# Performance work log

Measured on AMD Instinct MI355X. Metric: run time of the kernel, lower is better.

## Reference

```python
import jax, jax.numpy as jnp
import numpy as np

N_NODES = 100000
N_EDGES = 3200000
IN_Z = 32
PROJ_H = 64
LOOP_D = 32
DEC_H = 64


def setup_inputs() -> dict:
    key = jax.random.key(0)
    ks = jax.random.split(key, 10)
    z_mod = jax.random.normal(ks[0], (N_NODES, IN_Z), dtype=jnp.float32)
    edge_index = jax.random.randint(ks[1], (2, N_EDGES), 0, N_NODES, dtype=jnp.int64)
    # loop_proj: Linear(32->64), ReLU, Linear(64->32)
    w1 = jax.random.normal(ks[2], (IN_Z, PROJ_H), dtype=jnp.float32) / np.sqrt(IN_Z)
    b1 = jnp.zeros((PROJ_H,), dtype=jnp.float32)
    w2 = jax.random.normal(ks[3], (PROJ_H, LOOP_D), dtype=jnp.float32) / np.sqrt(PROJ_H)
    b2 = jnp.zeros((LOOP_D,), dtype=jnp.float32)
    # decoder: Linear(2*loop_dim -> dec_hidden), ReLU, Linear(dec_hidden -> 1)
    dw1 = jax.random.normal(ks[4], (2 * LOOP_D, DEC_H), dtype=jnp.float32) / np.sqrt(2 * LOOP_D)
    db1 = jnp.zeros((DEC_H,), dtype=jnp.float32)
    dw2 = jax.random.normal(ks[5], (DEC_H, 1), dtype=jnp.float32) / np.sqrt(DEC_H)
    db2 = jnp.zeros((1,), dtype=jnp.float32)
    return {"z_mod": z_mod, "edge_index": edge_index, "w1": w1, "b1": b1,
            "w2": w2, "b2": b2, "dw1": dw1, "db1": db1, "dw2": dw2, "db2": db2}


def reference(z_mod, edge_index, w1, b1, w2, b2, dw1, db1, dw2, db2):
    # loop_proj: z_mod -> z_loop  [N, loop_dim]
    h = jax.nn.relu(z_mod @ w1 + b1)
    z_loop = h @ w2 + b2
    # edge-wise decoder: gather, concat, MLP
    zi = z_loop[edge_index[0]]            # [E, loop_dim]
    zj = z_loop[edge_index[1]]            # [E, loop_dim]
    he = jnp.concatenate([zi, zj], axis=-1)  # [E, 2*loop_dim]
    he = jax.nn.relu(he @ dw1 + db1)         # [E, dec_hidden]
    logits = (he @ dw2 + db2)[..., 0]        # [E]
    return logits
```

## Files before the change

### kernel.cpp

```cpp
#include <hip/hip_runtime.h>


typedef short bfrag4 __attribute__((ext_vector_type(4)));
typedef short s16x8  __attribute__((ext_vector_type(8)));
typedef float f32x4v __attribute__((ext_vector_type(4)));

#define N_NODES 100000
#define N_EDGES 3200000

__device__ __forceinline__ unsigned short f2bf(float f) {
    unsigned int i = __float_as_uint(f);
    unsigned int r = i + 0x7FFFu + ((i >> 16) & 1u);
    return (unsigned short)(r >> 16);
}

__device__ __forceinline__ bfrag4 cvt4(float x0, float x1, float x2, float x3) {
    bfrag4 v;
    v[0] = (short)f2bf(x0);
    v[1] = (short)f2bf(x1);
    v[2] = (short)f2bf(x2);
    v[3] = (short)f2bf(x3);
    return v;
}

__global__ __launch_bounds__(256) void node_proj_kernel(
    const float* __restrict__ z_mod,
    const float* __restrict__ w1,
    const float* __restrict__ b1,
    const float* __restrict__ w2,
    const float* __restrict__ b2,
    unsigned short* __restrict__ z_loop)
{
    __shared__ unsigned short hbuf[4][16 * 72];

    const int tid  = threadIdx.x;
    const int wave = tid >> 6;
    const int lane = tid & 63;
    const int quad = lane >> 4;
    const int col  = lane & 15;

    bfrag4 bw1[2][4];
    float  bias1[4];
    for (int t = 0; t < 4; ++t) {
        const int n = col + 16 * t;
        for (int s = 0; s < 2; ++s)
            for (int j = 0; j < 4; ++j)
                bw1[s][t][j] = (short)f2bf(w1[(s * 16 + quad * 4 + j) * 64 + n]);
        bias1[t] = b1[n];
    }
    bfrag4 bw2[4][2];
    float  bias2[2];
    for (int t = 0; t < 2; ++t) {
        const int n = col + 16 * t;
        for (int s = 0; s < 4; ++s)
            for (int j = 0; j < 4; ++j)
                bw2[s][t][j] = (short)f2bf(w2[(s * 16 + quad * 4 + j) * 32 + n]);
        bias2[t] = b2[n];
    }

    unsigned short* hrow = &hbuf[wave][0];

    const int gwave  = blockIdx.x * 4 + wave;
    const int nwaves = gridDim.x * 4;
    const int ntiles = N_NODES / 16;

    for (int tile = gwave; tile < ntiles; tile += nwaves) {
        const int node0 = tile * 16;
        const float* zrow = z_mod + (size_t)(node0 + col) * 32;

        f32x4v za0 = *(const f32x4v*)(zrow + 0 * 16 + quad * 4);
        f32x4v za1 = *(const f32x4v*)(zrow + 1 * 16 + quad * 4);
        bfrag4 a10 = cvt4(za0[0], za0[1], za0[2], za0[3]);
        bfrag4 a11 = cvt4(za1[0], za1[1], za1[2], za1[3]);

        f32x4v acc[4];
        for (int t = 0; t < 4; ++t) {
            f32x4v c = {bias1[t], bias1[t], bias1[t], bias1[t]};
            c = __builtin_amdgcn_mfma_f32_16x16x16bf16_1k(a10, bw1[0][t], c, 0, 0, 0);
            c = __builtin_amdgcn_mfma_f32_16x16x16bf16_1k(a11, bw1[1][t], c, 0, 0, 0);
            acc[t] = c;
        }

        for (int t = 0; t < 4; ++t)
            for (int r = 0; r < 4; ++r) {
                float v = acc[t][r];
                v = v > 0.f ? v : 0.f;
                hrow[(quad * 4 + r) * 72 + (col + 16 * t)] = f2bf(v);
            }
        asm volatile("" ::: "memory");

        f32x4v acc2[2];
        for (int t = 0; t < 2; ++t)
            acc2[t] = (f32x4v){bias2[t], bias2[t], bias2[t], bias2[t]};
        for (int s = 0; s < 4; ++s) {
            bfrag4 a2 = *(const bfrag4*)(hrow + col * 72 + s * 16 + quad * 4);
            for (int t = 0; t < 2; ++t)
                acc2[t] = __builtin_amdgcn_mfma_f32_16x16x16bf16_1k(a2, bw2[s][t], acc2[t], 0, 0, 0);
        }
        asm volatile("" ::: "memory");

        for (int t = 0; t < 2; ++t)
            for (int r = 0; r < 4; ++r)
                z_loop[(size_t)(node0 + quad * 4 + r) * 32 + (col + 16 * t)] =
                    f2bf(acc2[t][r]);
    }
}

__global__ __launch_bounds__(256) void edge_dec_kernel(
    const int*            __restrict__ eidx,
    const unsigned short* __restrict__ z_loop,
    const float*          __restrict__ dw1,
    const float*          __restrict__ db1,
    const float*          __restrict__ dw2,
    const float*          __restrict__ db2,
    float* __restrict__ out)
{
    const int tid  = threadIdx.x;
    const int lane = tid & 63;
    const int quad = lane >> 4;
    const int col  = lane & 15;

    s16x8 aw[2][4];
    float bias1[4][4];
    float w2v[4][4];
    for (int mt = 0; mt < 4; ++mt) {
        const int h = 16 * mt + col;
        for (int s = 0; s < 2; ++s)
            for (int j = 0; j < 8; ++j)
                aw[s][mt][j] = (short)f2bf(dw1[(32 * s + quad * 8 + j) * 64 + h]);
        for (int r = 0; r < 4; ++r) {
            bias1[mt][r] = db1[16 * mt + quad * 4 + r];
            w2v[mt][r]   = dw2[16 * mt + quad * 4 + r];
        }
    }
    const float bias2 = db2[0];

    const int gwave  = blockIdx.x * 4 + (tid >> 6);
    const int nwaves = gridDim.x * 4;
    const int npairs = N_EDGES / 32;

    int sA = eidx[gwave * 32 + col];
    int sB = eidx[gwave * 32 + 16 + col];
    int dA = eidx[N_EDGES + gwave * 32 + col];
    int dB = eidx[N_EDGES + gwave * 32 + 16 + col];

    for (int p = gwave; p < npairs; p += nwaves) {
        const int e0 = p * 32;

        s16x8 gA0 = *(const s16x8*)(z_loop + (size_t)sA * 32 + quad * 8);
        s16x8 gA1 = *(const s16x8*)(z_loop + (size_t)dA * 32 + quad * 8);
        s16x8 gB0 = *(const s16x8*)(z_loop + (size_t)sB * 32 + quad * 8);
        s16x8 gB1 = *(const s16x8*)(z_loop + (size_t)dB * 32 + quad * 8);

        const int pn = p + nwaves;
        const int pc = pn < npairs ? pn : gwave;
        sA = eidx[pc * 32 + col];
        sB = eidx[pc * 32 + 16 + col];
        dA = eidx[N_EDGES + pc * 32 + col];
        dB = eidx[N_EDGES + pc * 32 + 16 + col];

        f32x4v accA[4], accB[4];
        for (int mt = 0; mt < 4; ++mt) {
            f32x4v c = {bias1[mt][0], bias1[mt][1], bias1[mt][2], bias1[mt][3]};
            c = __builtin_amdgcn_mfma_f32_16x16x32_bf16(aw[0][mt], gA0, c, 0, 0, 0);
            c = __builtin_amdgcn_mfma_f32_16x16x32_bf16(aw[1][mt], gA1, c, 0, 0, 0);
            accA[mt] = c;
        }
        for (int mt = 0; mt < 4; ++mt) {
            f32x4v c = {bias1[mt][0], bias1[mt][1], bias1[mt][2], bias1[mt][3]};
            c = __builtin_amdgcn_mfma_f32_16x16x32_bf16(aw[0][mt], gB0, c, 0, 0, 0);
            c = __builtin_amdgcn_mfma_f32_16x16x32_bf16(aw[1][mt], gB1, c, 0, 0, 0);
            accB[mt] = c;
        }

        float pA = 0.f, pB = 0.f;
        for (int mt = 0; mt < 4; ++mt)
            for (int r = 0; r < 4; ++r) {
                float vA = accA[mt][r]; vA = vA > 0.f ? vA : 0.f;
                float vB = accB[mt][r]; vB = vB > 0.f ? vB : 0.f;
                pA += vA * w2v[mt][r];
                pB += vB * w2v[mt][r];
            }
        pA += __shfl_xor(pA, 16, 64);
        pA += __shfl_xor(pA, 32, 64);
        pB += __shfl_xor(pB, 16, 64);
        pB += __shfl_xor(pB, 32, 64);

        if (lane < 32) {
            float v = (lane < 16 ? pA : pB) + bias2;
            out[e0 + lane] = v;
        }
    }
}

extern "C" void kernel_launch(void* const* d_in, const int* in_sizes, int n_in,
                              void* d_out, int out_size, void* d_ws, size_t ws_size,
                              hipStream_t stream) {
    const float* z_mod = (const float*)d_in[0];
    const int*   eidx  = (const int*)d_in[1];
    const float* w1    = (const float*)d_in[2];
    const float* b1    = (const float*)d_in[3];
    const float* w2    = (const float*)d_in[4];
    const float* b2    = (const float*)d_in[5];
    const float* dw1   = (const float*)d_in[6];
    const float* db1   = (const float*)d_in[7];
    const float* dw2   = (const float*)d_in[8];
    const float* db2   = (const float*)d_in[9];
    float*          out    = (float*)d_out;
    unsigned short* z_loop = (unsigned short*)d_ws;

    node_proj_kernel<<<512, 256, 0, stream>>>(z_mod, w1, b1, w2, b2, z_loop);
    edge_dec_kernel<<<2048, 256, 0, stream>>>(eidx, z_loop, dw1, db1, dw2, db2, out);
}
```

Before: 152.3 us.

## Quantize projected node embeddings to int8 with per-node scales for edge gathers

The node projection kernel now stores z_loop as int8 with a per-node absmax scale instead of bf16, staging the quantized rows through shared memory for a coalesced write. The edge decoder gathers 8-byte int8 chunks plus a scale per endpoint and dequantizes to bf16 in registers before the MFMA. This halves the bytes of the random embedding gathers, at the cost of extra ALU work for dequantization, an additional scale gather per endpoint, and reduced numerical precision.

```diff
diff --git a/kernel.cpp b/kernel.cpp
--- a/kernel.cpp
+++ b/kernel.cpp
@@ -23,13 +23,31 @@
     return v;
 }
 
+__device__ __forceinline__ s16x8 dq8(long g, float s) {
+    int lo = (int)g;
+    int hi = (int)(g >> 32);
+    s16x8 o;
+#pragma unroll
+    for (int j = 0; j < 4; ++j) {
+        int bj = (lo << (24 - 8 * j)) >> 24;
+        o[j] = (short)f2bf((float)bj * s);
+    }
+#pragma unroll
+    for (int j = 0; j < 4; ++j) {
+        int bj = (hi << (24 - 8 * j)) >> 24;
+        o[4 + j] = (short)f2bf((float)bj * s);
+    }
+    return o;
+}
+
 __global__ __launch_bounds__(256) void node_proj_kernel(
     const float* __restrict__ z_mod,
     const float* __restrict__ w1,
     const float* __restrict__ b1,
     const float* __restrict__ w2,
     const float* __restrict__ b2,
-    unsigned short* __restrict__ z_loop)
+    char*  __restrict__ z8,
+    float* __restrict__ scales)
 {
     __shared__ unsigned short hbuf[4][16 * 72];
 
@@ -99,20 +117,40 @@
         }
         asm volatile("" ::: "memory");
 
-        for (int t = 0; t < 2; ++t)
+        float am[4];
+        for (int r = 0; r < 4; ++r)
+            am[r] = fmaxf(fabsf(acc2[0][r]), fabsf(acc2[1][r]));
+        for (int mask = 1; mask <= 8; mask <<= 1)
             for (int r = 0; r < 4; ++r)
-                z_loop[(size_t)(node0 + quad * 4 + r) * 32 + (col + 16 * t)] =
-                    f2bf(acc2[t][r]);
+                am[r] = fmaxf(am[r], __shfl_xor(am[r], mask, 64));
+
+        char* hb = (char*)hrow;
+        for (int r = 0; r < 4; ++r) {
+            const float inv = 127.f / fmaxf(am[r], 1e-30f);
+            for (int t = 0; t < 2; ++t) {
+                int q = (int)rintf(acc2[t][r] * inv);
+                hb[(quad * 4 + r) * 32 + (col + 16 * t)] = (char)q;
+            }
+        }
+        if (col == 0)
+            for (int r = 0; r < 4; ++r)
+                scales[node0 + quad * 4 + r] = am[r] * (1.f / 127.f);
+        asm volatile("" ::: "memory");
+
+        *(unsigned long long*)(z8 + (size_t)node0 * 32 + lane * 8) =
+            *(const unsigned long long*)(hb + lane * 8);
+        asm volatile("" ::: "memory");
     }
 }
 
 __global__ __launch_bounds__(256) void edge_dec_kernel(
-    const int*            __restrict__ eidx,
-    const unsigned short* __restrict__ z_loop,
-    const float*          __restrict__ dw1,
-    const float*          __restrict__ db1,
-    const float*          __restrict__ dw2,
-    const float*          __restrict__ db2,
+    const int*   __restrict__ eidx,
+    const char*  __restrict__ z8,
+    const float* __restrict__ scales,
+    const float* __restrict__ dw1,
+    const float* __restrict__ db1,
+    const float* __restrict__ dw2,
+    const float* __restrict__ db2,
     float* __restrict__ out)
 {
     const int tid  = threadIdx.x;
@@ -121,16 +159,16 @@
     const int col  = lane & 15;
 
     s16x8 aw[2][4];
-    float bias1[4][4];
-    float w2v[4][4];
+    f32x4v bias1v[4];
+    float  w2v[4][4];
     for (int mt = 0; mt < 4; ++mt) {
         const int h = 16 * mt + col;
         for (int s = 0; s < 2; ++s)
             for (int j = 0; j < 8; ++j)
                 aw[s][mt][j] = (short)f2bf(dw1[(32 * s + quad * 8 + j) * 64 + h]);
         for (int r = 0; r < 4; ++r) {
-            bias1[mt][r] = db1[16 * mt + quad * 4 + r];
-            w2v[mt][r]   = dw2[16 * mt + quad * 4 + r];
+            bias1v[mt][r] = db1[16 * mt + quad * 4 + r];
+            w2v[mt][r]    = dw2[16 * mt + quad * 4 + r];
         }
     }
     const float bias2 = db2[0];
@@ -147,10 +185,14 @@
     for (int p = gwave; p < npairs; p += nwaves) {
         const int e0 = p * 32;
 
-        s16x8 gA0 = *(const s16x8*)(z_loop + (size_t)sA * 32 + quad * 8);
-        s16x8 gA1 = *(const s16x8*)(z_loop + (size_t)dA * 32 + quad * 8);
-        s16x8 gB0 = *(const s16x8*)(z_loop + (size_t)sB * 32 + quad * 8);
-        s16x8 gB1 = *(const s16x8*)(z_loop + (size_t)dB * 32 + quad * 8);
+        long gA0 = *(const long*)(z8 + ((size_t)sA << 5) + (quad << 3));
+        long gA1 = *(const long*)(z8 + ((size_t)dA << 5) + (quad << 3));
+        long gB0 = *(const long*)(z8 + ((size_t)sB << 5) + (quad << 3));
+        long gB1 = *(const long*)(z8 + ((size_t)dB << 5) + (quad << 3));
+        float scA0 = scales[sA];
+        float scA1 = scales[dA];
+        float scB0 = scales[sB];
+        float scB1 = scales[dB];
 
         const int pn = p + nwaves;
         const int pc = pn < npairs ? pn : gwave;
@@ -159,18 +201,19 @@
         dA = eidx[N_EDGES + pc * 32 + col];
         dB = eidx[N_EDGES + pc * 32 + 16 + col];
 
+        s16x8 fA0 = dq8(gA0, scA0);
+        s16x8 fA1 = dq8(gA1, scA1);
+        s16x8 fB0 = dq8(gB0, scB0);
+        s16x8 fB1 = dq8(gB1, scB1);
+
         f32x4v accA[4], accB[4];
         for (int mt = 0; mt < 4; ++mt) {
-            f32x4v c = {bias1[mt][0], bias1[mt][1], bias1[mt][2], bias1[mt][3]};
-            c = __builtin_amdgcn_mfma_f32_16x16x32_bf16(aw[0][mt], gA0, c, 0, 0, 0);
-            c = __builtin_amdgcn_mfma_f32_16x16x32_bf16(aw[1][mt], gA1, c, 0, 0, 0);
-            accA[mt] = c;
+            f32x4v c = __builtin_amdgcn_mfma_f32_16x16x32_bf16(aw[0][mt], fA0, bias1v[mt], 0, 0, 0);
+            accA[mt] = __builtin_amdgcn_mfma_f32_16x16x32_bf16(aw[1][mt], fA1, c, 0, 0, 0);
         }
         for (int mt = 0; mt < 4; ++mt) {
-            f32x4v c = {bias1[mt][0], bias1[mt][1], bias1[mt][2], bias1[mt][3]};
-            c = __builtin_amdgcn_mfma_f32_16x16x32_bf16(aw[0][mt], gB0, c, 0, 0, 0);
-            c = __builtin_amdgcn_mfma_f32_16x16x32_bf16(aw[1][mt], gB1, c, 0, 0, 0);
-            accB[mt] = c;
+            f32x4v c = __builtin_amdgcn_mfma_f32_16x16x32_bf16(aw[0][mt], fB0, bias1v[mt], 0, 0, 0);
+            accB[mt] = __builtin_amdgcn_mfma_f32_16x16x32_bf16(aw[1][mt], fB1, c, 0, 0, 0);
         }
 
         float pA = 0.f, pB = 0.f;
@@ -206,9 +249,11 @@
     const float* db1   = (const float*)d_in[7];
     const float* dw2   = (const float*)d_in[8];
     const float* db2   = (const float*)d_in[9];
-    float*          out    = (float*)d_out;
-    unsigned short* z_loop = (unsigned short*)d_ws;
-
-    node_proj_kernel<<<512, 256, 0, stream>>>(z_mod, w1, b1, w2, b2, z_loop);
-    edge_dec_kernel<<<2048, 256, 0, stream>>>(eidx, z_loop, dw1, db1, dw2, db2, out);
-}
+    float* out = (float*)d_out;
+
+    char*  z8     = (char*)d_ws;
+    float* scales = (float*)((char*)d_ws + (size_t)N_NODES * 32);
+
+    node_proj_kernel<<<512, 256, 0, stream>>>(z_mod, w1, b1, w2, b2, z8, scales);
+    edge_dec_kernel<<<2048, 256, 0, stream>>>(eidx, z8, scales, dw1, db1, dw2, db2, out);
+}
```

Result: slower. 173.5 us (+13.9%).
